# Kernel optimization log

Hardware: AMD Instinct MI355X
Metric: run time of the kernel (lower is better)

## Reference

```python
import jax, jax.numpy as jnp
import numpy as np

N_NODES = 100000
DIM = 256
N_SAMPLES = 64
N_CLASSES = 10


def setup_inputs() -> dict:
    key = jax.random.key(0)
    k1, k2, k3 = jax.random.split(key, 3)
    data = jax.random.normal(k1, (N_SAMPLES, DIM), dtype=jnp.float32)
    V = jax.random.uniform(k2, (N_NODES, DIM), dtype=jnp.float32)  # node matrix (torch.rand init)
    labels = jax.random.randint(k3, (N_SAMPLES,), 0, N_CLASSES)
    return {"data": data, "V": V, "labels": labels, "it": 0}


def reference(data, V, labels, it):
    # SOINN+ per-sample BMU search + BMU/sBMU weight pull, fixed node capacity.
    # eps schedules exactly as in ASOINN.forward.
    eps_b = 1.0 / (it + 2)
    eps_n = 1.0 / ((it + 1) * 100)

    def step(Vc, sample):
        # pairwise L2 distance of sample vs all nodes: [N]
        diff = sample[None, :] - Vc
        dists = jnp.sqrt(jnp.sum(diff * diff, axis=-1) + 1e-12)
        neg_vals, idx = jax.lax.top_k(-dists, 2)  # two smallest
        b, s = idx[0], idx[1]
        # update_bmu: V[b] += eps_b * (sample - V[b]); neighbor pull on sBMU
        Vc = Vc.at[b].add(eps_b * (sample - Vc[b]))
        Vc = Vc.at[s].add(eps_n * (sample - Vc[s]))
        return Vc, -neg_vals  # (b_dist, s_dist)

    V_final, bmu_dists = jax.lax.scan(step, V, data)
    return bmu_dists  # [N_SAMPLES, 2]
```

## Files before the change

### kernel.cpp

```cpp
#include <hip/hip_runtime.h>
#include <math.h>


#define N_NODES 100000
#define DIM     256
#define NS      64
#define NCH     1563
#define KC      32
#define NBMW    3125
#define CAP     4096
#define KL      192
#define KLS     136

typedef unsigned long long u64;

__device__ __forceinline__ u64 pk(float d, int i) {
  return ((u64)__float_as_uint(d) << 32) | (unsigned)i;
}
__device__ __forceinline__ u64 tkey(float d, int slot, int node) {
  return ((u64)__float_as_uint(d) << 32) |
         (u64)(0x80000000u | ((unsigned)slot << 17) | (unsigned)node);
}
__device__ __forceinline__ u64 umin64(u64 a, u64 b) { return a < b ? a : b; }
__device__ __forceinline__ u64 umax64(u64 a, u64 b) { return a > b ? a : b; }
__device__ __forceinline__ void mrg2(u64& A0, u64& A1, u64 B0, u64 B1) {
  u64 m = umax64(A0, B0);
  A0 = umin64(A0, B0);
  A1 = umin64(umin64(A1, B1), m);
}

template <int C>
__device__ __forceinline__ u64 dpp64(u64 x) {
  unsigned lo = (unsigned)__builtin_amdgcn_update_dpp(
      (int)0xFFFFFFFF, (int)(unsigned)(x & 0xFFFFFFFFull), C, 0xF, 0xF, false);
  unsigned hi = (unsigned)__builtin_amdgcn_update_dpp(
      (int)0xFFFFFFFF, (int)(unsigned)(x >> 32), C, 0xF, 0xF, false);
  return ((u64)hi << 32) | lo;
}
template <int C>
__device__ __forceinline__ void dpp_round(u64& A0, u64& A1) {
  u64 B0 = dpp64<C>(A0);
  u64 B1 = dpp64<C>(A1);
  mrg2(A0, A1, B0, B1);
}

__global__ void k_xx(const float* __restrict__ X, float* __restrict__ XX) {
  int i = blockIdx.x, j = threadIdx.x;
  const float* xi = X + i * DIM;
  const float* xj = X + j * DIM;
  float acc = 0.f;
  for (int k = 0; k < DIM; k += 4) {
    float4 a = *(const float4*)(xi + k);
    float4 b = *(const float4*)(xj + k);
    acc += a.x * b.x + a.y * b.y + a.z * b.z + a.w * b.w;
  }
  XX[i * NS + j] = acc;
}

__global__ __launch_bounds__(256) void k_dist(const float* __restrict__ X,
                                              const float* __restrict__ V,
                                              const float* __restrict__ XX,
                                              float* __restrict__ P,
                                              float* __restrict__ PT,
                                              float* __restrict__ Q,
                                              u64* __restrict__ SUMC) {
  __shared__ float Xl[KC][68];
  __shared__ float Vl[KC][132];
  __shared__ float sq[128];
  const int tid = threadIdx.x;
  const int n0  = blockIdx.x * 128;
  const int ty  = tid >> 5;
  const int tx  = tid & 31;
  float acc[8][4];
#pragma unroll
  for (int i = 0; i < 8; i++)
#pragma unroll
    for (int u = 0; u < 4; u++) acc[i][u] = 0.f;
  float qa = 0.f;
  const int xsl = tid & 63;
  const int xkk = (tid >> 6) * 8;
  const int vn  = tid & 127;
  const int vkk = (tid >> 7) * 16;
  const bool vok = (n0 + vn < N_NODES);
  const float* vrow = V + (size_t)(n0 + vn) * DIM + vkk;
  const float* xrow = X + xsl * DIM + xkk;

  float4 xr0, xr1, vr[4];
  xr0 = *(const float4*)(xrow + 0);
  xr1 = *(const float4*)(xrow + 4);
#pragma unroll
  for (int m = 0; m < 4; m++)
    vr[m] = vok ? *(const float4*)(vrow + 4 * m) : make_float4(0.f, 0.f, 0.f, 0.f);

  for (int c = 0; c < 8; c++) {
    __syncthreads();
    Xl[xkk + 0][xsl] = xr0.x; Xl[xkk + 1][xsl] = xr0.y;
    Xl[xkk + 2][xsl] = xr0.z; Xl[xkk + 3][xsl] = xr0.w;
    Xl[xkk + 4][xsl] = xr1.x; Xl[xkk + 5][xsl] = xr1.y;
    Xl[xkk + 6][xsl] = xr1.z; Xl[xkk + 7][xsl] = xr1.w;
#pragma unroll
    for (int m = 0; m < 4; m++) {
      Vl[vkk + 4 * m + 0][vn] = vr[m].x; Vl[vkk + 4 * m + 1][vn] = vr[m].y;
      Vl[vkk + 4 * m + 2][vn] = vr[m].z; Vl[vkk + 4 * m + 3][vn] = vr[m].w;
    }
    __syncthreads();
    if (c + 1 < 8) {
      int kc = (c + 1) * KC;
      xr0 = *(const float4*)(xrow + kc);
      xr1 = *(const float4*)(xrow + kc + 4);
#pragma unroll
      for (int m = 0; m < 4; m++)
        vr[m] = vok ? *(const float4*)(vrow + kc + 4 * m)
                    : make_float4(0.f, 0.f, 0.f, 0.f);
    }
    if (tid < 128) {
      float qq = 0.f;
#pragma unroll 8
      for (int k = 0; k < KC; k++) { float t = Vl[k][tid]; qq += t * t; }
      qa += qq;
    }
#pragma unroll 4
    for (int k = 0; k < KC; k++) {
      float xs[8], vs[4];
      *(float4*)&xs[0] = *(const float4*)&Xl[k][ty * 8];
      *(float4*)&xs[4] = *(const float4*)&Xl[k][ty * 8 + 4];
      *(float4*)&vs[0] = *(const float4*)&Vl[k][tx * 4];
#pragma unroll
      for (int i = 0; i < 8; i++)
#pragma unroll
        for (int u = 0; u < 4; u++) acc[i][u] += xs[i] * vs[u];
    }
  }
  if (tid < 128) sq[tid] = qa;
  __syncthreads();
  if (tid < 128 && n0 + tid < N_NODES) Q[n0 + tid] = qa;
  float qs[4];
  *(float4*)&qs[0] = *(const float4*)&sq[tx * 4];
  const bool full = (n0 + 128) <= N_NODES;
#pragma unroll
  for (int i = 0; i < 8; i++) {
    int s = ty * 8 + i;
    float xn = XX[s * NS + s];
#pragma unroll
    for (int u = 0; u < 4; u++) acc[i][u] = xn - 2.f * acc[i][u] + qs[u];
    float* prow = P + (size_t)s * N_NODES + n0 + tx * 4;
    if (full) {
      *(float4*)(prow) = make_float4(acc[i][0], acc[i][1], acc[i][2], acc[i][3]);
    } else {
#pragma unroll
      for (int u = 0; u < 4; u++) {
        int n = n0 + tx * 4 + u;
        if (n < N_NODES) prow[u] = acc[i][u];
      }
    }
  }
#pragma unroll
  for (int u = 0; u < 4; u++) {
    int n = n0 + tx * 4 + u;
    if (n < N_NODES) {
      float* pt = PT + (size_t)n * NS + ty * 8;
      *(float4*)(pt)     = make_float4(acc[0][u], acc[1][u], acc[2][u], acc[3][u]);
      *(float4*)(pt + 4) = make_float4(acc[4][u], acc[5][u], acc[6][u], acc[7][u]);
    }
  }
#pragma unroll
  for (int i = 0; i < 8; i++) {
    int s = ty * 8 + i;
    u64 key = ~0ull;
#pragma unroll
    for (int u = 0; u < 4; u++) {
      int n = n0 + tx * 4 + u;
      if (n < N_NODES) key = umin64(key, pk(acc[i][u], n));
    }
#pragma unroll
    for (int off = 1; off <= 8; off <<= 1)
      key = umin64(key, (u64)__shfl_xor((unsigned long long)key, off, 64));
    if ((tx & 15) == 0) {
      int chunk = (n0 >> 6) + (tx >> 4);
      if (chunk < NCH) SUMC[(size_t)s * NCH + chunk] = key;
    }
  }
}

__global__ __launch_bounds__(1024) void k_build(const u64* __restrict__ SUMC,
                                                const float* __restrict__ P,
                                                u64* __restrict__ L) {
  __shared__ u64 A[CAP];
  __shared__ u64 Twave[16];
  __shared__ float Tsh;
  __shared__ int cnt;
  const int j = blockIdx.x, tid = threadIdx.x;
  const int w = tid >> 6, l = tid & 63;
  {
    int base = w * 98;
    u64 v0 = (base + l < NCH) ? SUMC[(size_t)j * NCH + base + l] : ~0ull;
    u64 v1 = (l < 34 && base + 64 + l < NCH)
                 ? SUMC[(size_t)j * NCH + base + 64 + l] : ~0ull;
    u64 s9 = ~0ull;
#pragma unroll
    for (int r = 0; r < 9; r++) {
      u64 m = umin64(v0, v1);
#pragma unroll
      for (int off = 1; off <= 32; off <<= 1)
        m = umin64(m, (u64)__shfl_xor((unsigned long long)m, off, 64));
      if (r == 8) { s9 = m; } else {
        if (v0 == m) v0 = ~0ull;
        if (v1 == m) v1 = ~0ull;
      }
    }
    if (l == 0) Twave[w] = s9;
  }
  __syncthreads();
  if (tid == 0) {
    u64 t = 0;
    for (int i = 0; i < 16; i++) t = umax64(t, Twave[i]);
    Tsh = __uint_as_float((unsigned)(t >> 32));
    cnt = 0;
  }
  __syncthreads();
  const float T = Tsh;
  const float* prow = P + (size_t)j * N_NODES;
  for (int n0 = tid * 4; n0 < N_NODES + 3; n0 += 4096) {
    float d[4];
    if (n0 + 3 < N_NODES) {
      float4 p = *(const float4*)(prow + n0);
      d[0] = p.x; d[1] = p.y; d[2] = p.z; d[3] = p.w;
    } else {
#pragma unroll
      for (int e = 0; e < 4; e++)
        d[e] = (n0 + e < N_NODES) ? prow[n0 + e] : INFINITY;
    }
#pragma unroll
    for (int e = 0; e < 4; e++) {
      if (d[e] <= T) {
        int pos = atomicAdd(&cnt, 1);
        if (pos < CAP) A[pos] = pk(d[e], n0 + e);
      }
    }
  }
  __syncthreads();
  int n = cnt; if (n > CAP) n = CAP;
  int M = 256; while (M < n) M <<= 1;
  for (int i = tid; i < M; i += 1024)
    if (i >= n) A[i] = ~0ull;
  __syncthreads();
  for (int k = 2; k <= M; k <<= 1)
    for (int s2 = k >> 1; s2 > 0; s2 >>= 1) {
      for (int i = tid; i < M; i += 1024) {
        int p = i ^ s2;
        if (p > i) {
          u64 a = A[i], b = A[p];
          bool up = ((i & k) == 0);
          if ((a > b) == up) { A[i] = b; A[p] = a; }
        }
      }
      __syncthreads();
    }
  for (int i = tid; i < KLS; i += 1024) L[(size_t)j * KL + i] = A[i];
}

__global__ __launch_bounds__(192) void k_seq(
    const float* __restrict__ PT, const float* __restrict__ Q,
    const float* __restrict__ XXg, const u64* __restrict__ L,
    const int* __restrict__ itp, float* __restrict__ out) {
  __shared__ float XXl[NS * 65];
  __shared__ float g[128][65];
  __shared__ float qv[128];
  __shared__ unsigned int bitmap[NBMW];
  __shared__ int tracked[128];
  __shared__ u64 cand16[NS][16];
  __shared__ float specg[4][6][NS];
  __shared__ float specq[4][6];
  __shared__ int   specid[4][6];
  __shared__ int readyC[NS];
  __shared__ int readyS[NS];
  __shared__ int done[NS];

  const int tid = threadIdx.x;
  const int wv = tid >> 6;
  const int lane = tid & 63;

  for (int i = tid; i < NS * NS; i += 192) {
    int r = i >> 6, c = i & 63;
    XXl[r * 65 + c] = XXg[i];
  }
  for (int i = tid; i < NBMW; i += 192) bitmap[i] = 0u;
  for (int i = tid; i < NS; i += 192) { readyC[i] = 0; readyS[i] = 0; done[i] = 0; }
  __syncthreads();

  const int it = itp[0];
  const float eps_b = 1.0f / (float)(it + 2);
  const float eps_n = 1.0f / (float)((it + 1) * 100);
  const float xdl = XXl[lane * 65 + lane];

  if (wv == 0) {
    int ns = 0;
    int pw0 = -1, pw1 = -1, pw2 = -1, pw3 = -1;
    for (int j = 0; j < NS; j++) {
      while (__hip_atomic_load(&readyC[j], __ATOMIC_ACQUIRE,
                               __HIP_MEMORY_SCOPE_WORKGROUP) == 0)
        __builtin_amdgcn_s_sleep(1);
      const int sb = j & 3;
      u64 ck = (lane < 16) ? cand16[j][lane] : ~0ull;
      float gA = g[lane][j], gB = g[lane + 64][j];
      float qvA = qv[lane],  qvB = qv[lane + 64];
      int   tA = tracked[lane], tB = tracked[lane + 64];
      float xrow = XXl[j * 65 + lane];
      float xnj  = XXl[j * 65 + j];
      u64 A0 = ~0ull, A1 = ~0ull;
      {
        int id = (int)(unsigned)(ck & 0xFFFFFFFFull);
        bool ok = (ck != ~0ull) && id != pw0 && id != pw1 && id != pw2 && id != pw3;
        if (ok) { A0 = ck; }
      }
      if (lane < ns)      { float d = xnj - 2.f * gA + qvA; mrg2(A0, A1, tkey(d, lane, tA), ~0ull); }
      if (lane + 64 < ns) { float d = xnj - 2.f * gB + qvB; mrg2(A0, A1, tkey(d, lane + 64, tB), ~0ull); }
      dpp_round<0x111>(A0, A1);
      dpp_round<0x112>(A0, A1);
      dpp_round<0x114>(A0, A1);
      dpp_round<0x118>(A0, A1);
      dpp_round<0x142>(A0, A1);
      dpp_round<0x143>(A0, A1);
      const unsigned lo0 = (unsigned)__builtin_amdgcn_readlane(
          (int)(unsigned)(A0 & 0xFFFFFFFFull), 63);
      const unsigned lo1 = (unsigned)__builtin_amdgcn_readlane(
          (int)(unsigned)(A1 & 0xFFFFFFFFull), 63);
      const int r0 = (int)(lo0 & 0x1FFFFu);
      const int r1 = (int)(lo1 & 0x1FFFFu);
      const bool new0 = (lo0 & 0x80000000u) == 0u;
      const bool new1 = (lo1 & 0x80000000u) == 0u;
      const int sl0 = new0 ? ns : (int)((lo0 >> 17) & 127u);
      const int sl1 = new1 ? (ns + (new0 ? 1 : 0)) : (int)((lo1 >> 17) & 127u);
      if (lane == 63) {
        float2 o;
        o.x = sqrtf(fmaxf(__uint_as_float((unsigned)(A0 >> 32)), 0.f) + 1e-12f);
        o.y = sqrtf(fmaxf(__uint_as_float((unsigned)(A1 >> 32)), 0.f) + 1e-12f);
        *(float2*)(out + j * 2) = o;
      }
      float gt0 = g[sl0][lane];
      float gt1 = g[sl1][lane];
      while (__hip_atomic_load(&readyS[j], __ATOMIC_ACQUIRE,
                               __HIP_MEMORY_SCOPE_WORKGROUP) == 0)
        __builtin_amdgcn_s_sleep(1);
      float sgv[6], sqv[6]; int sid[6];
#pragma unroll
      for (int s = 0; s < 6; s++) {
        sgv[s] = specg[sb][s][lane];
        sid[s] = specid[sb][s];
        sqv[s] = specq[sb][s];
      }
      bool hit0 = false, hit1 = false;
      float pv0 = 0.f, qq0 = 0.f, pv1 = 0.f, qq1 = 0.f;
#pragma unroll
      for (int s = 0; s < 6; s++) {
        bool h0 = (sid[s] == r0), h1 = (sid[s] == r1);
        pv0 = h0 ? sgv[s] : pv0;  qq0 = h0 ? sqv[s] : qq0;  hit0 |= h0;
        pv1 = h1 ? sgv[s] : pv1;  qq1 = h1 ? sqv[s] : qq1;  hit1 |= h1;
      }
      if (new0 && !hit0) { pv0 = PT[(size_t)r0 * NS + lane]; qq0 = Q[r0]; }
      if (new1 && !hit1) { pv1 = PT[(size_t)r1 * NS + lane]; qq1 = Q[r1]; }
      float gold0 = new0 ? (0.5f * (xdl + qq0 - pv0)) : gt0;
      float qold0 = new0 ? qq0
                         : __uint_as_float((unsigned)__builtin_amdgcn_readlane(
                               (int)__float_as_uint(sl0 < 64 ? qvA : qvB), sl0 & 63));
      float gj0 = __uint_as_float(
          (unsigned)__builtin_amdgcn_readlane((int)__float_as_uint(gold0), j));
      g[sl0][lane] = (1.f - eps_b) * gold0 + eps_b * xrow;
      if (lane == 0) {
        float om = 1.f - eps_b;
        qv[sl0] = om * om * qold0 + 2.f * eps_b * om * gj0 + eps_b * eps_b * xnj;
        tracked[sl0] = r0;
        if (new0) bitmap[r0 >> 5] |= 1u << (r0 & 31);
      }
      float gold1 = new1 ? (0.5f * (xdl + qq1 - pv1)) : gt1;
      float qold1 = new1 ? qq1
                         : __uint_as_float((unsigned)__builtin_amdgcn_readlane(
                               (int)__float_as_uint(sl1 < 64 ? qvA : qvB), sl1 & 63));
      float gj1 = __uint_as_float(
          (unsigned)__builtin_amdgcn_readlane((int)__float_as_uint(gold1), j));
      g[sl1][lane] = (1.f - eps_n) * gold1 + eps_n * xrow;
      if (lane == 0) {
        float on = 1.f - eps_n;
        qv[sl1] = on * on * qold1 + 2.f * eps_n * on * gj1 + eps_n * eps_n * xnj;
        tracked[sl1] = r1;
        if (new1) bitmap[r1 >> 5] |= 1u << (r1 & 31);
      }
      ns += (new0 ? 1 : 0) + (new1 ? 1 : 0);
      pw2 = pw0; pw3 = pw1; pw0 = r0; pw1 = r1;
      __hip_atomic_store(&done[j], 1, __ATOMIC_RELEASE,
                         __HIP_MEMORY_SCOPE_WORKGROUP);
    }
  } else {
    for (int t = (wv == 1 ? 0 : 1); t < NS; t += 2) {
      const u64* Lr = L + (size_t)t * KL;
      u64 e0 = Lr[lane], e1 = Lr[lane + 64];
      u64 e2 = (lane < 8) ? Lr[128 + lane] : ~0ull;
      if (t >= 3) {
        while (__hip_atomic_load(&done[t - 3], __ATOMIC_ACQUIRE,
                                 __HIP_MEMORY_SCOPE_WORKGROUP) == 0)
          __builtin_amdgcn_s_sleep(1);
      }
      int i0 = (int)(unsigned)(e0 & 0xFFFFFFFFull);
      int i1 = (int)(unsigned)(e1 & 0xFFFFFFFFull);
      int i2 = (int)(unsigned)(e2 & 0xFFFFFFFFull);
      bool t0 = (e0 == ~0ull) || ((bitmap[i0 >> 5] >> (i0 & 31)) & 1u);
      bool t1 = (e1 == ~0ull) || ((bitmap[i1 >> 5] >> (i1 & 31)) & 1u);
      bool t2 = (e2 == ~0ull) || ((bitmap[i2 >> 5] >> (i2 & 31)) & 1u);
      u64 um0 = ~__ballot(t0), um1 = ~__ballot(t1), um2 = ~__ballot(t2);
      u64 below = (1ull << lane) - 1;
      int c0n = __popcll((unsigned long long)um0);
      int c1n = __popcll((unsigned long long)um1);
      int rank0 = __popcll((unsigned long long)(um0 & below));
      int rank1 = c0n + __popcll((unsigned long long)(um1 & below));
      int rank2 = c0n + c1n + __popcll((unsigned long long)(um2 & below));
      if (!t0 && rank0 < 16) cand16[t][rank0] = e0;
      if (!t1 && rank1 < 16) cand16[t][rank1] = e1;
      if (!t2 && rank2 < 16) cand16[t][rank2] = e2;
      int U = c0n + c1n + __popcll((unsigned long long)um2);
      if (lane < 16 && lane >= U) cand16[t][lane] = ~0ull;
      __hip_atomic_store(&readyC[t], 1, __ATOMIC_RELEASE,
                         __HIP_MEMORY_SCOPE_WORKGROUP);
      const int sb = t & 3;
      int ids[6];
#pragma unroll
      for (int s = 0; s < 6; s++)
        ids[s] = (int)(unsigned)(cand16[t][s] & 0xFFFFFFFFull);
#pragma unroll
      for (int s = 0; s < 6; s++)
        specg[sb][s][lane] = PT[(size_t)ids[s] * NS + lane];
      if (lane < 6) {
        specid[sb][lane] = ids[lane];
        specq[sb][lane] = Q[ids[lane]];
      }
      __hip_atomic_store(&readyS[t], 1, __ATOMIC_RELEASE,
                         __HIP_MEMORY_SCOPE_WORKGROUP);
    }
  }
}

extern "C" void kernel_launch(void* const* d_in, const int* in_sizes, int n_in,
                              void* d_out, int out_size, void* d_ws, size_t ws_size,
                              hipStream_t stream) {
  const float* X  = (const float*)d_in[0];
  const float* V  = (const float*)d_in[1];
  const int*  itp = (const int*)d_in[3];
  float* out = (float*)d_out;

  char* ws = (char*)d_ws;
  size_t off = 0;
  auto alloc = [&](size_t bytes) -> void* {
    size_t o = (off + 255) & ~(size_t)255;
    off = o + bytes;
    return (void*)(ws + o);
  };
  float* P    = (float*)alloc((size_t)NS * N_NODES * sizeof(float));
  float* PT   = (float*)alloc((size_t)NS * N_NODES * sizeof(float));
  float* Q    = (float*)alloc((size_t)N_NODES * sizeof(float));
  float* XXp  = (float*)alloc((size_t)NS * NS * sizeof(float));
  u64*   SUMC = (u64*)alloc((size_t)NS * NCH * sizeof(u64));
  u64*   Lst  = (u64*)alloc((size_t)NS * KL * sizeof(u64));

  k_xx   <<<NS, NS, 0, stream>>>(X, XXp);
  k_dist <<<(N_NODES + 127) / 128, 256, 0, stream>>>(X, V, XXp, P, PT, Q, SUMC);
  k_build<<<NS, 1024, 0, stream>>>(SUMC, P, Lst);
  k_seq  <<<1, 192, 0, stream>>>(PT, Q, XXp, Lst, itp, out);
}
```

Baseline: 308.1 us.

## Deepen k_seq producer pipeline and keep tracked state in registers

The sequential BMU kernel now uses four producer waves instead of two, with an 8-deep speculation buffer holding 12 prefetched candidate rows instead of 6. The consumer wave keeps per-slot q and tracked ids in registers, and prefetches the next step's g column, forwarding this step's updates by readlane. It also signals done earlier, right after setting the bitmap, so producers can run further ahead. The rank is encoded in the candidate key, so a speculative row is found by direct indexing rather than an id search. The exclusion window grows to 10 previous winners to match the deeper lookahead. The aim is to shorten the serial critical path per sample, at the cost of more shared memory and more complex forwarding logic.

```diff
diff --git a/kernel.cpp b/kernel.cpp
--- a/kernel.cpp
+++ b/kernel.cpp
@@ -28,6 +28,10 @@
   A0 = umin64(A0, B0);
   A1 = umin64(umin64(A1, B1), m);
 }
+__device__ __forceinline__ float rdlane_f(float v, int l) {
+  return __uint_as_float((unsigned)__builtin_amdgcn_readlane(
+      (int)__float_as_uint(v), l));
+}
 
 template <int C>
 __device__ __forceinline__ u64 dpp64(u64 x) {
@@ -43,6 +47,11 @@
   u64 B1 = dpp64<C>(A1);
   mrg2(A0, A1, B0, B1);
 }
+
+#define SPIN(flag)                                                        \
+  while (__hip_atomic_load(&(flag), __ATOMIC_ACQUIRE,                     \
+                           __HIP_MEMORY_SCOPE_WORKGROUP) == 0)            \
+    __builtin_amdgcn_s_sleep(1);
 
 __global__ void k_xx(const float* __restrict__ X, float* __restrict__ XX) {
   int i = blockIdx.x, j = threadIdx.x;
@@ -259,19 +268,16 @@
   for (int i = tid; i < KLS; i += 1024) L[(size_t)j * KL + i] = A[i];
 }
 
-__global__ __launch_bounds__(192) void k_seq(
+__global__ __launch_bounds__(320) void k_seq(
     const float* __restrict__ PT, const float* __restrict__ Q,
     const float* __restrict__ XXg, const u64* __restrict__ L,
     const int* __restrict__ itp, float* __restrict__ out) {
   __shared__ float XXl[NS * 65];
   __shared__ float g[128][65];
-  __shared__ float qv[128];
   __shared__ unsigned int bitmap[NBMW];
-  __shared__ int tracked[128];
   __shared__ u64 cand16[NS][16];
-  __shared__ float specg[4][6][NS];
-  __shared__ float specq[4][6];
-  __shared__ int   specid[4][6];
+  __shared__ float specg[8][12][NS];
+  __shared__ float specq[8][12];
   __shared__ int readyC[NS];
   __shared__ int readyS[NS];
   __shared__ int done[NS];
@@ -280,38 +286,51 @@
   const int wv = tid >> 6;
   const int lane = tid & 63;
 
-  for (int i = tid; i < NS * NS; i += 192) {
+  for (int i = tid; i < NS * NS; i += 320) {
     int r = i >> 6, c = i & 63;
     XXl[r * 65 + c] = XXg[i];
   }
-  for (int i = tid; i < NBMW; i += 192) bitmap[i] = 0u;
-  for (int i = tid; i < NS; i += 192) { readyC[i] = 0; readyS[i] = 0; done[i] = 0; }
+  for (int i = tid; i < NBMW; i += 320) bitmap[i] = 0u;
+  for (int i = tid; i < NS; i += 320) { readyC[i] = 0; readyS[i] = 0; done[i] = 0; }
   __syncthreads();
 
   const int it = itp[0];
   const float eps_b = 1.0f / (float)(it + 2);
   const float eps_n = 1.0f / (float)((it + 1) * 100);
-  const float xdl = XXl[lane * 65 + lane];
 
   if (wv == 0) {
+    const float xdl = XXl[lane * 65 + lane];
+    float gA = 0.f, gB = 0.f;
+    float qvA = 0.f, qvB = 0.f;
+    int tA = 0, tB = 0;
     int ns = 0;
-    int pw0 = -1, pw1 = -1, pw2 = -1, pw3 = -1;
+    int pw[10];
+#pragma unroll
+    for (int k2 = 0; k2 < 10; k2++) pw[k2] = -1;
+
+    SPIN(readyC[0]);
+    SPIN(readyC[1]);
+    u64 ck = (lane < 16) ? cand16[0][lane] : ~0ull;
+    SPIN(readyS[0]);
+
     for (int j = 0; j < NS; j++) {
-      while (__hip_atomic_load(&readyC[j], __ATOMIC_ACQUIRE,
-                               __HIP_MEMORY_SCOPE_WORKGROUP) == 0)
-        __builtin_amdgcn_s_sleep(1);
-      const int sb = j & 3;
-      u64 ck = (lane < 16) ? cand16[j][lane] : ~0ull;
-      float gA = g[lane][j], gB = g[lane + 64][j];
-      float qvA = qv[lane],  qvB = qv[lane + 64];
-      int   tA = tracked[lane], tB = tracked[lane + 64];
-      float xrow = XXl[j * 65 + lane];
-      float xnj  = XXl[j * 65 + j];
+      u64 ckn = ~0ull;
+      float gAn = 0.f, gBn = 0.f;
+      if (j < 63) {
+        if (lane < 16) ckn = cand16[j + 1][lane];
+        gAn = g[lane][j + 1];
+        gBn = g[lane + 64][j + 1];
+      }
+      float xrowv = XXl[j * 65 + lane];
+      const float xnj = rdlane_f(xdl, j);
+
       u64 A0 = ~0ull, A1 = ~0ull;
       {
-        int id = (int)(unsigned)(ck & 0xFFFFFFFFull);
-        bool ok = (ck != ~0ull) && id != pw0 && id != pw1 && id != pw2 && id != pw3;
-        if (ok) { A0 = ck; }
+        int id = (int)((unsigned)ck & 0x1FFFFu);
+        bool ok = (ck != ~0ull);
+#pragma unroll
+        for (int k2 = 0; k2 < 10; k2++) ok = ok && (id != pw[k2]);
+        if (ok) A0 = ck;
       }
       if (lane < ns)      { float d = xnj - 2.f * gA + qvA; mrg2(A0, A1, tkey(d, lane, tA), ~0ull); }
       if (lane + 64 < ns) { float d = xnj - 2.f * gB + qvB; mrg2(A0, A1, tkey(d, lane + 64, tB), ~0ull); }
@@ -331,75 +350,87 @@
       const bool new1 = (lo1 & 0x80000000u) == 0u;
       const int sl0 = new0 ? ns : (int)((lo0 >> 17) & 127u);
       const int sl1 = new1 ? (ns + (new0 ? 1 : 0)) : (int)((lo1 >> 17) & 127u);
+      const int rk0 = (int)((lo0 >> 17) & 15u);
+      const int rk1 = (int)((lo1 >> 17) & 15u);
+
+      float gt0 = g[sl0][lane];
+      float gt1 = g[sl1][lane];
+      const int sb = j & 7;
+      float pv0 = 0.f, qq0 = 0.f, pv1 = 0.f, qq1 = 0.f;
+      if (new0) { pv0 = specg[sb][rk0][lane]; qq0 = specq[sb][rk0]; }
+      if (new1) { pv1 = specg[sb][rk1][lane]; qq1 = specq[sb][rk1]; }
+
+      if (lane == 0) {
+        if (new0) bitmap[r0 >> 5] |= 1u << (r0 & 31);
+        if (new1) bitmap[r1 >> 5] |= 1u << (r1 & 31);
+      }
+      __hip_atomic_store(&done[j], 1, __ATOMIC_RELEASE,
+                         __HIP_MEMORY_SCOPE_WORKGROUP);
+
       if (lane == 63) {
         float2 o;
         o.x = sqrtf(fmaxf(__uint_as_float((unsigned)(A0 >> 32)), 0.f) + 1e-12f);
         o.y = sqrtf(fmaxf(__uint_as_float((unsigned)(A1 >> 32)), 0.f) + 1e-12f);
         *(float2*)(out + j * 2) = o;
       }
-      float gt0 = g[sl0][lane];
-      float gt1 = g[sl1][lane];
-      while (__hip_atomic_load(&readyS[j], __ATOMIC_ACQUIRE,
-                               __HIP_MEMORY_SCOPE_WORKGROUP) == 0)
-        __builtin_amdgcn_s_sleep(1);
-      float sgv[6], sqv[6]; int sid[6];
-#pragma unroll
-      for (int s = 0; s < 6; s++) {
-        sgv[s] = specg[sb][s][lane];
-        sid[s] = specid[sb][s];
-        sqv[s] = specq[sb][s];
-      }
-      bool hit0 = false, hit1 = false;
-      float pv0 = 0.f, qq0 = 0.f, pv1 = 0.f, qq1 = 0.f;
-#pragma unroll
-      for (int s = 0; s < 6; s++) {
-        bool h0 = (sid[s] == r0), h1 = (sid[s] == r1);
-        pv0 = h0 ? sgv[s] : pv0;  qq0 = h0 ? sqv[s] : qq0;  hit0 |= h0;
-        pv1 = h1 ? sgv[s] : pv1;  qq1 = h1 ? sqv[s] : qq1;  hit1 |= h1;
-      }
-      if (new0 && !hit0) { pv0 = PT[(size_t)r0 * NS + lane]; qq0 = Q[r0]; }
-      if (new1 && !hit1) { pv1 = PT[(size_t)r1 * NS + lane]; qq1 = Q[r1]; }
+
+      if (new0 && rk0 >= 12) { pv0 = PT[(size_t)r0 * NS + lane]; qq0 = Q[r0]; }
+      if (new1 && rk1 >= 12) { pv1 = PT[(size_t)r1 * NS + lane]; qq1 = Q[r1]; }
+
       float gold0 = new0 ? (0.5f * (xdl + qq0 - pv0)) : gt0;
-      float qold0 = new0 ? qq0
-                         : __uint_as_float((unsigned)__builtin_amdgcn_readlane(
-                               (int)__float_as_uint(sl0 < 64 ? qvA : qvB), sl0 & 63));
-      float gj0 = __uint_as_float(
-          (unsigned)__builtin_amdgcn_readlane((int)__float_as_uint(gold0), j));
-      g[sl0][lane] = (1.f - eps_b) * gold0 + eps_b * xrow;
-      if (lane == 0) {
-        float om = 1.f - eps_b;
-        qv[sl0] = om * om * qold0 + 2.f * eps_b * om * gj0 + eps_b * eps_b * xnj;
-        tracked[sl0] = r0;
-        if (new0) bitmap[r0 >> 5] |= 1u << (r0 & 31);
-      }
+      float gnew0 = (1.f - eps_b) * gold0 + eps_b * xrowv;
+      g[sl0][lane] = gnew0;
+      float qold0 = new0 ? qq0 : rdlane_f(sl0 < 64 ? qvA : qvB, sl0 & 63);
+      float gj0 = rdlane_f(gold0, j);
+      float om = 1.f - eps_b;
+      float qn0 = om * om * qold0 + 2.f * eps_b * om * gj0 + eps_b * eps_b * xnj;
+
       float gold1 = new1 ? (0.5f * (xdl + qq1 - pv1)) : gt1;
-      float qold1 = new1 ? qq1
-                         : __uint_as_float((unsigned)__builtin_amdgcn_readlane(
-                               (int)__float_as_uint(sl1 < 64 ? qvA : qvB), sl1 & 63));
-      float gj1 = __uint_as_float(
-          (unsigned)__builtin_amdgcn_readlane((int)__float_as_uint(gold1), j));
-      g[sl1][lane] = (1.f - eps_n) * gold1 + eps_n * xrow;
-      if (lane == 0) {
-        float on = 1.f - eps_n;
-        qv[sl1] = on * on * qold1 + 2.f * eps_n * on * gj1 + eps_n * eps_n * xnj;
-        tracked[sl1] = r1;
-        if (new1) bitmap[r1 >> 5] |= 1u << (r1 & 31);
-      }
+      float gnew1 = (1.f - eps_n) * gold1 + eps_n * xrowv;
+      g[sl1][lane] = gnew1;
+      float qold1 = new1 ? qq1 : rdlane_f(sl1 < 64 ? qvA : qvB, sl1 & 63);
+      float gj1 = rdlane_f(gold1, j);
+      float on = 1.f - eps_n;
+      float qn1 = on * on * qold1 + 2.f * eps_n * on * gj1 + eps_n * eps_n * xnj;
+
+      if (sl0 < 64) { if (lane == sl0)      { qvA = qn0; tA = r0; } }
+      else          { if (lane == sl0 - 64) { qvB = qn0; tB = r0; } }
+      if (sl1 < 64) { if (lane == sl1)      { qvA = qn1; tA = r1; } }
+      else          { if (lane == sl1 - 64) { qvB = qn1; tB = r1; } }
+
+      if (j < 63) {
+        float xnext = rdlane_f(xrowv, j + 1);
+        float xd1 = rdlane_f(xdl, j + 1);
+        float goldn0 = new0 ? (0.5f * (xd1 + qq0 - rdlane_f(pv0, j + 1)))
+                            : rdlane_f(sl0 < 64 ? gAn : gBn, sl0 & 63);
+        float gp0 = (1.f - eps_b) * goldn0 + eps_b * xnext;
+        float goldn1 = new1 ? (0.5f * (xd1 + qq1 - rdlane_f(pv1, j + 1)))
+                            : rdlane_f(sl1 < 64 ? gAn : gBn, sl1 & 63);
+        float gp1 = (1.f - eps_n) * goldn1 + eps_n * xnext;
+        if (sl0 < 64) { if (lane == sl0)      gAn = gp0; }
+        else          { if (lane == sl0 - 64) gBn = gp0; }
+        if (sl1 < 64) { if (lane == sl1)      gAn = gp1; }
+        else          { if (lane == sl1 - 64) gBn = gp1; }
+        gA = gAn; gB = gBn;
+      }
+
       ns += (new0 ? 1 : 0) + (new1 ? 1 : 0);
-      pw2 = pw0; pw3 = pw1; pw0 = r0; pw1 = r1;
-      __hip_atomic_store(&done[j], 1, __ATOMIC_RELEASE,
-                         __HIP_MEMORY_SCOPE_WORKGROUP);
+#pragma unroll
+      for (int k2 = 9; k2 >= 2; k2--) pw[k2] = pw[k2 - 2];
+      pw[0] = r0; pw[1] = r1;
+
+      if (j < 63) {
+        SPIN(readyS[j + 1]);
+        if (j < 62) SPIN(readyC[j + 2]);
+        ck = ckn;
+      }
     }
   } else {
-    for (int t = (wv == 1 ? 0 : 1); t < NS; t += 2) {
+    for (int t = wv - 1; t < NS; t += 4) {
       const u64* Lr = L + (size_t)t * KL;
       u64 e0 = Lr[lane], e1 = Lr[lane + 64];
       u64 e2 = (lane < 8) ? Lr[128 + lane] : ~0ull;
-      if (t >= 3) {
-        while (__hip_atomic_load(&done[t - 3], __ATOMIC_ACQUIRE,
-                                 __HIP_MEMORY_SCOPE_WORKGROUP) == 0)
-          __builtin_amdgcn_s_sleep(1);
-      }
+      if (t >= 6) { SPIN(done[t - 6]); }
       int i0 = (int)(unsigned)(e0 & 0xFFFFFFFFull);
       int i1 = (int)(unsigned)(e1 & 0xFFFFFFFFull);
       int i2 = (int)(unsigned)(e2 & 0xFFFFFFFFull);
@@ -413,25 +444,24 @@
       int rank0 = __popcll((unsigned long long)(um0 & below));
       int rank1 = c0n + __popcll((unsigned long long)(um1 & below));
       int rank2 = c0n + c1n + __popcll((unsigned long long)(um2 & below));
-      if (!t0 && rank0 < 16) cand16[t][rank0] = e0;
-      if (!t1 && rank1 < 16) cand16[t][rank1] = e1;
-      if (!t2 && rank2 < 16) cand16[t][rank2] = e2;
+      if (!t0 && rank0 < 16) cand16[t][rank0] = e0 | ((u64)(unsigned)rank0 << 17);
+      if (!t1 && rank1 < 16) cand16[t][rank1] = e1 | ((u64)(unsigned)rank1 << 17);
+      if (!t2 && rank2 < 16) cand16[t][rank2] = e2 | ((u64)(unsigned)rank2 << 17);
       int U = c0n + c1n + __popcll((unsigned long long)um2);
       if (lane < 16 && lane >= U) cand16[t][lane] = ~0ull;
       __hip_atomic_store(&readyC[t], 1, __ATOMIC_RELEASE,
                          __HIP_MEMORY_SCOPE_WORKGROUP);
-      const int sb = t & 3;
-      int ids[6];
-#pragma unroll
-      for (int s = 0; s < 6; s++)
-        ids[s] = (int)(unsigned)(cand16[t][s] & 0xFFFFFFFFull);
-#pragma unroll
-      for (int s = 0; s < 6; s++)
+      const int sb = t & 7;
+      int ids[12];
+#pragma unroll
+      for (int s = 0; s < 12; s++) {
+        u64 e = cand16[t][s];
+        ids[s] = (e == ~0ull) ? 0 : (int)((unsigned)e & 0x1FFFFu);
+      }
+#pragma unroll
+      for (int s = 0; s < 12; s++)
         specg[sb][s][lane] = PT[(size_t)ids[s] * NS + lane];
-      if (lane < 6) {
-        specid[sb][lane] = ids[lane];
-        specq[sb][lane] = Q[ids[lane]];
-      }
+      if (lane < 12) specq[sb][lane] = Q[ids[lane]];
       __hip_atomic_store(&readyS[t], 1, __ATOMIC_RELEASE,
                          __HIP_MEMORY_SCOPE_WORKGROUP);
     }
@@ -463,5 +493,5 @@
   k_xx   <<<NS, NS, 0, stream>>>(X, XXp);
   k_dist <<<(N_NODES + 127) / 128, 256, 0, stream>>>(X, V, XXp, P, PT, Q, SUMC);
   k_build<<<NS, 1024, 0, stream>>>(SUMC, P, Lst);
-  k_seq  <<<1, 192, 0, stream>>>(PT, Q, XXp, Lst, itp, out);
-}
+  k_seq  <<<1, 320, 0, stream>>>(PT, Q, XXp, Lst, itp, out);
+}
```

Measured after the change: 329.9 us. 1.07x slower.

## Encode candidate rank in key and signal done earlier in sequential loop

Applied to the files above, without the earlier changes.

The serial wave now reads each candidate's prefetch slot straight from bits packed into its key, instead of matching ids against the speculative slots. This drops the specid table and the separate readyC flag in favour of one readyS wait. The done flag is published right after the bitmap update, so helper waves can start filtering sooner. Next-iteration shared loads are hoisted to the end of the loop, and xnj now comes from a readlane. The risk is that the rank bits overlap node-id bits when ids are masked to 17 bits, and that waiting on readyS makes the serial wave stall on the PT prefetch.

```diff
diff --git a/kernel.cpp b/kernel.cpp
--- a/kernel.cpp
+++ b/kernel.cpp
@@ -28,6 +28,10 @@
   A0 = umin64(A0, B0);
   A1 = umin64(umin64(A1, B1), m);
 }
+__device__ __forceinline__ float rdlane_f(float v, int l) {
+  return __uint_as_float((unsigned)__builtin_amdgcn_readlane(
+      (int)__float_as_uint(v), l));
+}
 
 template <int C>
 __device__ __forceinline__ u64 dpp64(u64 x) {
@@ -43,6 +47,11 @@
   u64 B1 = dpp64<C>(A1);
   mrg2(A0, A1, B0, B1);
 }
+
+#define SPIN(flag)                                                        \
+  while (__hip_atomic_load(&(flag), __ATOMIC_ACQUIRE,                     \
+                           __HIP_MEMORY_SCOPE_WORKGROUP) == 0)            \
+    __builtin_amdgcn_s_sleep(1);
 
 __global__ void k_xx(const float* __restrict__ X, float* __restrict__ XX) {
   int i = blockIdx.x, j = threadIdx.x;
@@ -271,8 +280,6 @@
   __shared__ u64 cand16[NS][16];
   __shared__ float specg[4][6][NS];
   __shared__ float specq[4][6];
-  __shared__ int   specid[4][6];
-  __shared__ int readyC[NS];
   __shared__ int readyS[NS];
   __shared__ int done[NS];
 
@@ -285,7 +292,7 @@
     XXl[r * 65 + c] = XXg[i];
   }
   for (int i = tid; i < NBMW; i += 192) bitmap[i] = 0u;
-  for (int i = tid; i < NS; i += 192) { readyC[i] = 0; readyS[i] = 0; done[i] = 0; }
+  for (int i = tid; i < NS; i += 192) { readyS[i] = 0; done[i] = 0; }
   __syncthreads();
 
   const int it = itp[0];
@@ -296,22 +303,20 @@
   if (wv == 0) {
     int ns = 0;
     int pw0 = -1, pw1 = -1, pw2 = -1, pw3 = -1;
+    SPIN(readyS[0]);
+    u64 ck = (lane < 16) ? cand16[0][lane] : ~0ull;
+    float gA = g[lane][0], gB = g[lane + 64][0];
+    float qvA = qv[lane], qvB = qv[lane + 64];
+    int tA = tracked[lane], tB = tracked[lane + 64];
+    float xrow = XXl[0 * 65 + lane];
+
     for (int j = 0; j < NS; j++) {
-      while (__hip_atomic_load(&readyC[j], __ATOMIC_ACQUIRE,
-                               __HIP_MEMORY_SCOPE_WORKGROUP) == 0)
-        __builtin_amdgcn_s_sleep(1);
-      const int sb = j & 3;
-      u64 ck = (lane < 16) ? cand16[j][lane] : ~0ull;
-      float gA = g[lane][j], gB = g[lane + 64][j];
-      float qvA = qv[lane],  qvB = qv[lane + 64];
-      int   tA = tracked[lane], tB = tracked[lane + 64];
-      float xrow = XXl[j * 65 + lane];
-      float xnj  = XXl[j * 65 + j];
+      const float xnj = rdlane_f(xdl, j);
       u64 A0 = ~0ull, A1 = ~0ull;
       {
-        int id = (int)(unsigned)(ck & 0xFFFFFFFFull);
+        int id = (int)((unsigned)ck & 0x1FFFFu);
         bool ok = (ck != ~0ull) && id != pw0 && id != pw1 && id != pw2 && id != pw3;
-        if (ok) { A0 = ck; }
+        if (ok) A0 = ck;
       }
       if (lane < ns)      { float d = xnj - 2.f * gA + qvA; mrg2(A0, A1, tkey(d, lane, tA), ~0ull); }
       if (lane + 64 < ns) { float d = xnj - 2.f * gB + qvB; mrg2(A0, A1, tkey(d, lane + 64, tB), ~0ull); }
@@ -331,75 +336,69 @@
       const bool new1 = (lo1 & 0x80000000u) == 0u;
       const int sl0 = new0 ? ns : (int)((lo0 >> 17) & 127u);
       const int sl1 = new1 ? (ns + (new0 ? 1 : 0)) : (int)((lo1 >> 17) & 127u);
+      const int rk0 = (int)((lo0 >> 17) & 15u);
+      const int rk1 = (int)((lo1 >> 17) & 15u);
+
+      const int sb = j & 3;
+      float gt0 = g[sl0][lane];
+      float gt1 = g[sl1][lane];
+      float pv0 = 0.f, qq0 = 0.f, pv1 = 0.f, qq1 = 0.f;
+      if (new0) { pv0 = specg[sb][rk0][lane]; qq0 = specq[sb][rk0]; }
+      if (new1) { pv1 = specg[sb][rk1][lane]; qq1 = specq[sb][rk1]; }
+
+      if (lane == 0) {
+        if (new0) bitmap[r0 >> 5] |= 1u << (r0 & 31);
+        if (new1) bitmap[r1 >> 5] |= 1u << (r1 & 31);
+      }
+      __hip_atomic_store(&done[j], 1, __ATOMIC_RELEASE,
+                         __HIP_MEMORY_SCOPE_WORKGROUP);
+
       if (lane == 63) {
         float2 o;
         o.x = sqrtf(fmaxf(__uint_as_float((unsigned)(A0 >> 32)), 0.f) + 1e-12f);
         o.y = sqrtf(fmaxf(__uint_as_float((unsigned)(A1 >> 32)), 0.f) + 1e-12f);
         *(float2*)(out + j * 2) = o;
       }
-      float gt0 = g[sl0][lane];
-      float gt1 = g[sl1][lane];
-      while (__hip_atomic_load(&readyS[j], __ATOMIC_ACQUIRE,
-                               __HIP_MEMORY_SCOPE_WORKGROUP) == 0)
-        __builtin_amdgcn_s_sleep(1);
-      float sgv[6], sqv[6]; int sid[6];
-#pragma unroll
-      for (int s = 0; s < 6; s++) {
-        sgv[s] = specg[sb][s][lane];
-        sid[s] = specid[sb][s];
-        sqv[s] = specq[sb][s];
-      }
-      bool hit0 = false, hit1 = false;
-      float pv0 = 0.f, qq0 = 0.f, pv1 = 0.f, qq1 = 0.f;
-#pragma unroll
-      for (int s = 0; s < 6; s++) {
-        bool h0 = (sid[s] == r0), h1 = (sid[s] == r1);
-        pv0 = h0 ? sgv[s] : pv0;  qq0 = h0 ? sqv[s] : qq0;  hit0 |= h0;
-        pv1 = h1 ? sgv[s] : pv1;  qq1 = h1 ? sqv[s] : qq1;  hit1 |= h1;
-      }
-      if (new0 && !hit0) { pv0 = PT[(size_t)r0 * NS + lane]; qq0 = Q[r0]; }
-      if (new1 && !hit1) { pv1 = PT[(size_t)r1 * NS + lane]; qq1 = Q[r1]; }
+
+      if (new0 && rk0 >= 6) { pv0 = PT[(size_t)r0 * NS + lane]; qq0 = Q[r0]; }
+      if (new1 && rk1 >= 6) { pv1 = PT[(size_t)r1 * NS + lane]; qq1 = Q[r1]; }
+
       float gold0 = new0 ? (0.5f * (xdl + qq0 - pv0)) : gt0;
-      float qold0 = new0 ? qq0
-                         : __uint_as_float((unsigned)__builtin_amdgcn_readlane(
-                               (int)__float_as_uint(sl0 < 64 ? qvA : qvB), sl0 & 63));
-      float gj0 = __uint_as_float(
-          (unsigned)__builtin_amdgcn_readlane((int)__float_as_uint(gold0), j));
       g[sl0][lane] = (1.f - eps_b) * gold0 + eps_b * xrow;
+      float qold0 = new0 ? qq0 : rdlane_f(sl0 < 64 ? qvA : qvB, sl0 & 63);
+      float gj0 = rdlane_f(gold0, j);
       if (lane == 0) {
         float om = 1.f - eps_b;
         qv[sl0] = om * om * qold0 + 2.f * eps_b * om * gj0 + eps_b * eps_b * xnj;
         tracked[sl0] = r0;
-        if (new0) bitmap[r0 >> 5] |= 1u << (r0 & 31);
       }
       float gold1 = new1 ? (0.5f * (xdl + qq1 - pv1)) : gt1;
-      float qold1 = new1 ? qq1
-                         : __uint_as_float((unsigned)__builtin_amdgcn_readlane(
-                               (int)__float_as_uint(sl1 < 64 ? qvA : qvB), sl1 & 63));
-      float gj1 = __uint_as_float(
-          (unsigned)__builtin_amdgcn_readlane((int)__float_as_uint(gold1), j));
       g[sl1][lane] = (1.f - eps_n) * gold1 + eps_n * xrow;
+      float qold1 = new1 ? qq1 : rdlane_f(sl1 < 64 ? qvA : qvB, sl1 & 63);
+      float gj1 = rdlane_f(gold1, j);
       if (lane == 0) {
         float on = 1.f - eps_n;
         qv[sl1] = on * on * qold1 + 2.f * eps_n * on * gj1 + eps_n * eps_n * xnj;
         tracked[sl1] = r1;
-        if (new1) bitmap[r1 >> 5] |= 1u << (r1 & 31);
       }
       ns += (new0 ? 1 : 0) + (new1 ? 1 : 0);
       pw2 = pw0; pw3 = pw1; pw0 = r0; pw1 = r1;
-      __hip_atomic_store(&done[j], 1, __ATOMIC_RELEASE,
-                         __HIP_MEMORY_SCOPE_WORKGROUP);
+
+      if (j < 63) {
+        SPIN(readyS[j + 1]);
+        ck = (lane < 16) ? cand16[j + 1][lane] : ~0ull;
+        gA = g[lane][j + 1]; gB = g[lane + 64][j + 1];
+        qvA = qv[lane]; qvB = qv[lane + 64];
+        tA = tracked[lane]; tB = tracked[lane + 64];
+        xrow = XXl[(j + 1) * 65 + lane];
+      }
     }
   } else {
     for (int t = (wv == 1 ? 0 : 1); t < NS; t += 2) {
       const u64* Lr = L + (size_t)t * KL;
       u64 e0 = Lr[lane], e1 = Lr[lane + 64];
       u64 e2 = (lane < 8) ? Lr[128 + lane] : ~0ull;
-      if (t >= 3) {
-        while (__hip_atomic_load(&done[t - 3], __ATOMIC_ACQUIRE,
-                                 __HIP_MEMORY_SCOPE_WORKGROUP) == 0)
-          __builtin_amdgcn_s_sleep(1);
-      }
+      if (t >= 3) { SPIN(done[t - 3]); }
       int i0 = (int)(unsigned)(e0 & 0xFFFFFFFFull);
       int i1 = (int)(unsigned)(e1 & 0xFFFFFFFFull);
       int i2 = (int)(unsigned)(e2 & 0xFFFFFFFFull);
@@ -413,25 +412,20 @@
       int rank0 = __popcll((unsigned long long)(um0 & below));
       int rank1 = c0n + __popcll((unsigned long long)(um1 & below));
       int rank2 = c0n + c1n + __popcll((unsigned long long)(um2 & below));
-      if (!t0 && rank0 < 16) cand16[t][rank0] = e0;
-      if (!t1 && rank1 < 16) cand16[t][rank1] = e1;
-      if (!t2 && rank2 < 16) cand16[t][rank2] = e2;
+      if (!t0 && rank0 < 16) cand16[t][rank0] = e0 | ((u64)(unsigned)rank0 << 17);
+      if (!t1 && rank1 < 16) cand16[t][rank1] = e1 | ((u64)(unsigned)rank1 << 17);
+      if (!t2 && rank2 < 16) cand16[t][rank2] = e2 | ((u64)(unsigned)rank2 << 17);
       int U = c0n + c1n + __popcll((unsigned long long)um2);
       if (lane < 16 && lane >= U) cand16[t][lane] = ~0ull;
-      __hip_atomic_store(&readyC[t], 1, __ATOMIC_RELEASE,
-                         __HIP_MEMORY_SCOPE_WORKGROUP);
       const int sb = t & 3;
       int ids[6];
 #pragma unroll
       for (int s = 0; s < 6; s++)
-        ids[s] = (int)(unsigned)(cand16[t][s] & 0xFFFFFFFFull);
+        ids[s] = (int)((unsigned)cand16[t][s] & 0x1FFFFu);
 #pragma unroll
       for (int s = 0; s < 6; s++)
         specg[sb][s][lane] = PT[(size_t)ids[s] * NS + lane];
-      if (lane < 6) {
-        specid[sb][lane] = ids[lane];
-        specq[sb][lane] = Q[ids[lane]];
-      }
+      if (lane < 6) specq[sb][lane] = Q[ids[lane]];
       __hip_atomic_store(&readyS[t], 1, __ATOMIC_RELEASE,
                          __HIP_MEMORY_SCOPE_WORKGROUP);
     }
```

After: 309.6 us. Within noise of the previous version (+0.5%).

## Halve distance-kernel node tile and use packed FP32 FMA inner loop

Applied to the files above, without the earlier changes.

The distance GEMM block now covers 64 nodes instead of 128, so each thread computes an 8x2 tile and the grid doubles to 1563 blocks. The inner product uses inline v_pk_fma_f32 with op_sel to broadcast sample values, so one instruction performs two FMAs. The V tile load is reorganized so four threads cover each node row, and the chunk-min reduction now spans a full 32-lane group, with one SUMC entry written per block. The aim is more blocks for occupancy across the MI355X CUs plus higher FMA throughput. The cost is lower data reuse per thread and more shared-memory traffic per FLOP.

```diff
diff --git a/kernel.cpp b/kernel.cpp
--- a/kernel.cpp
+++ b/kernel.cpp
@@ -13,6 +13,7 @@
 #define KLS     136
 
 typedef unsigned long long u64;
+typedef __attribute__((ext_vector_type(2))) float f32x2;
 
 __device__ __forceinline__ u64 pk(float d, int i) {
   return ((u64)__float_as_uint(d) << 32) | (unsigned)i;
@@ -27,6 +28,15 @@
   u64 m = umax64(A0, B0);
   A0 = umin64(A0, B0);
   A1 = umin64(umin64(A1, B1), m);
+}
+
+__device__ __forceinline__ void pkfma_lo(f32x2& acc, f32x2 xp, f32x2 vp) {
+  asm("v_pk_fma_f32 %0, %1, %2, %0 op_sel:[0,0,0] op_sel_hi:[0,1,1]"
+      : "+v"(acc) : "v"(xp), "v"(vp));
+}
+__device__ __forceinline__ void pkfma_hi(f32x2& acc, f32x2 xp, f32x2 vp) {
+  asm("v_pk_fma_f32 %0, %1, %2, %0 op_sel:[1,0,0] op_sel_hi:[1,1,1]"
+      : "+v"(acc) : "v"(xp), "v"(vp));
 }
 
 template <int C>
@@ -65,32 +75,29 @@
                                               float* __restrict__ Q,
                                               u64* __restrict__ SUMC) {
   __shared__ float Xl[KC][68];
-  __shared__ float Vl[KC][132];
-  __shared__ float sq[128];
+  __shared__ float Vl[KC][66];
+  __shared__ float sq[64];
   const int tid = threadIdx.x;
-  const int n0  = blockIdx.x * 128;
+  const int n0  = blockIdx.x * 64;
   const int ty  = tid >> 5;
   const int tx  = tid & 31;
-  float acc[8][4];
-#pragma unroll
-  for (int i = 0; i < 8; i++)
-#pragma unroll
-    for (int u = 0; u < 4; u++) acc[i][u] = 0.f;
+  f32x2 acc2[8];
+#pragma unroll
+  for (int i = 0; i < 8; i++) { acc2[i][0] = 0.f; acc2[i][1] = 0.f; }
   float qa = 0.f;
   const int xsl = tid & 63;
   const int xkk = (tid >> 6) * 8;
-  const int vn  = tid & 127;
-  const int vkk = (tid >> 7) * 16;
-  const bool vok = (n0 + vn < N_NODES);
-  const float* vrow = V + (size_t)(n0 + vn) * DIM + vkk;
+  const int vrw = tid >> 2;
+  const int vkk = (tid & 3) * 8;
+  const bool vok = (n0 + vrw < N_NODES);
+  const float* vrow = V + (size_t)(n0 + vrw) * DIM + vkk;
   const float* xrow = X + xsl * DIM + xkk;
 
-  float4 xr0, xr1, vr[4];
+  float4 xr0, xr1, vr0, vr1;
   xr0 = *(const float4*)(xrow + 0);
   xr1 = *(const float4*)(xrow + 4);
-#pragma unroll
-  for (int m = 0; m < 4; m++)
-    vr[m] = vok ? *(const float4*)(vrow + 4 * m) : make_float4(0.f, 0.f, 0.f, 0.f);
+  vr0 = vok ? *(const float4*)(vrow + 0) : make_float4(0.f, 0.f, 0.f, 0.f);
+  vr1 = vok ? *(const float4*)(vrow + 4) : make_float4(0.f, 0.f, 0.f, 0.f);
 
   for (int c = 0; c < 8; c++) {
     __syncthreads();
@@ -98,22 +105,19 @@
     Xl[xkk + 2][xsl] = xr0.z; Xl[xkk + 3][xsl] = xr0.w;
     Xl[xkk + 4][xsl] = xr1.x; Xl[xkk + 5][xsl] = xr1.y;
     Xl[xkk + 6][xsl] = xr1.z; Xl[xkk + 7][xsl] = xr1.w;
-#pragma unroll
-    for (int m = 0; m < 4; m++) {
-      Vl[vkk + 4 * m + 0][vn] = vr[m].x; Vl[vkk + 4 * m + 1][vn] = vr[m].y;
-      Vl[vkk + 4 * m + 2][vn] = vr[m].z; Vl[vkk + 4 * m + 3][vn] = vr[m].w;
-    }
+    Vl[vkk + 0][vrw] = vr0.x; Vl[vkk + 1][vrw] = vr0.y;
+    Vl[vkk + 2][vrw] = vr0.z; Vl[vkk + 3][vrw] = vr0.w;
+    Vl[vkk + 4][vrw] = vr1.x; Vl[vkk + 5][vrw] = vr1.y;
+    Vl[vkk + 6][vrw] = vr1.z; Vl[vkk + 7][vrw] = vr1.w;
     __syncthreads();
     if (c + 1 < 8) {
       int kc = (c + 1) * KC;
       xr0 = *(const float4*)(xrow + kc);
       xr1 = *(const float4*)(xrow + kc + 4);
-#pragma unroll
-      for (int m = 0; m < 4; m++)
-        vr[m] = vok ? *(const float4*)(vrow + kc + 4 * m)
-                    : make_float4(0.f, 0.f, 0.f, 0.f);
-    }
-    if (tid < 128) {
+      vr0 = vok ? *(const float4*)(vrow + kc) : make_float4(0.f, 0.f, 0.f, 0.f);
+      vr1 = vok ? *(const float4*)(vrow + kc + 4) : make_float4(0.f, 0.f, 0.f, 0.f);
+    }
+    if (tid < 64) {
       float qq = 0.f;
 #pragma unroll 8
       for (int k = 0; k < KC; k++) { float t = Vl[k][tid]; qq += t * t; }
@@ -121,42 +125,53 @@
     }
 #pragma unroll 4
     for (int k = 0; k < KC; k++) {
-      float xs[8], vs[4];
-      *(float4*)&xs[0] = *(const float4*)&Xl[k][ty * 8];
-      *(float4*)&xs[4] = *(const float4*)&Xl[k][ty * 8 + 4];
-      *(float4*)&vs[0] = *(const float4*)&Vl[k][tx * 4];
-#pragma unroll
-      for (int i = 0; i < 8; i++)
-#pragma unroll
-        for (int u = 0; u < 4; u++) acc[i][u] += xs[i] * vs[u];
-    }
-  }
-  if (tid < 128) sq[tid] = qa;
-  __syncthreads();
-  if (tid < 128 && n0 + tid < N_NODES) Q[n0 + tid] = qa;
-  float qs[4];
-  *(float4*)&qs[0] = *(const float4*)&sq[tx * 4];
-  const bool full = (n0 + 128) <= N_NODES;
+      float4 xa = *(const float4*)&Xl[k][ty * 8];
+      float4 xb = *(const float4*)&Xl[k][ty * 8 + 4];
+      f32x2 vp = *(const f32x2*)&Vl[k][tx * 2];
+      f32x2 xp0, xp1, xp2, xp3;
+      xp0[0] = xa.x; xp0[1] = xa.y;
+      xp1[0] = xa.z; xp1[1] = xa.w;
+      xp2[0] = xb.x; xp2[1] = xb.y;
+      xp3[0] = xb.z; xp3[1] = xb.w;
+      pkfma_lo(acc2[0], xp0, vp);
+      pkfma_hi(acc2[1], xp0, vp);
+      pkfma_lo(acc2[2], xp1, vp);
+      pkfma_hi(acc2[3], xp1, vp);
+      pkfma_lo(acc2[4], xp2, vp);
+      pkfma_hi(acc2[5], xp2, vp);
+      pkfma_lo(acc2[6], xp3, vp);
+      pkfma_hi(acc2[7], xp3, vp);
+    }
+  }
+  float acc[8][2];
+#pragma unroll
+  for (int i = 0; i < 8; i++) { acc[i][0] = acc2[i][0]; acc[i][1] = acc2[i][1]; }
+  if (tid < 64) sq[tid] = qa;
+  __syncthreads();
+  if (tid < 64 && n0 + tid < N_NODES) Q[n0 + tid] = qa;
+  float qs[2];
+  *(f32x2*)&qs[0] = *(const f32x2*)&sq[tx * 2];
+  const bool full = (n0 + 64) <= N_NODES;
 #pragma unroll
   for (int i = 0; i < 8; i++) {
     int s = ty * 8 + i;
     float xn = XX[s * NS + s];
 #pragma unroll
-    for (int u = 0; u < 4; u++) acc[i][u] = xn - 2.f * acc[i][u] + qs[u];
-    float* prow = P + (size_t)s * N_NODES + n0 + tx * 4;
+    for (int u = 0; u < 2; u++) acc[i][u] = xn - 2.f * acc[i][u] + qs[u];
+    float* prow = P + (size_t)s * N_NODES + n0 + tx * 2;
     if (full) {
-      *(float4*)(prow) = make_float4(acc[i][0], acc[i][1], acc[i][2], acc[i][3]);
+      *(float2*)(prow) = make_float2(acc[i][0], acc[i][1]);
     } else {
 #pragma unroll
-      for (int u = 0; u < 4; u++) {
-        int n = n0 + tx * 4 + u;
+      for (int u = 0; u < 2; u++) {
+        int n = n0 + tx * 2 + u;
         if (n < N_NODES) prow[u] = acc[i][u];
       }
     }
   }
 #pragma unroll
-  for (int u = 0; u < 4; u++) {
-    int n = n0 + tx * 4 + u;
+  for (int u = 0; u < 2; u++) {
+    int n = n0 + tx * 2 + u;
     if (n < N_NODES) {
       float* pt = PT + (size_t)n * NS + ty * 8;
       *(float4*)(pt)     = make_float4(acc[0][u], acc[1][u], acc[2][u], acc[3][u]);
@@ -168,17 +183,14 @@
     int s = ty * 8 + i;
     u64 key = ~0ull;
 #pragma unroll
-    for (int u = 0; u < 4; u++) {
-      int n = n0 + tx * 4 + u;
+    for (int u = 0; u < 2; u++) {
+      int n = n0 + tx * 2 + u;
       if (n < N_NODES) key = umin64(key, pk(acc[i][u], n));
     }
 #pragma unroll
-    for (int off = 1; off <= 8; off <<= 1)
+    for (int off = 1; off <= 16; off <<= 1)
       key = umin64(key, (u64)__shfl_xor((unsigned long long)key, off, 64));
-    if ((tx & 15) == 0) {
-      int chunk = (n0 >> 6) + (tx >> 4);
-      if (chunk < NCH) SUMC[(size_t)s * NCH + chunk] = key;
-    }
+    if (tx == 0) SUMC[(size_t)s * NCH + blockIdx.x] = key;
   }
 }
 
@@ -461,7 +473,7 @@
   u64*   Lst  = (u64*)alloc((size_t)NS * KL * sizeof(u64));
 
   k_xx   <<<NS, NS, 0, stream>>>(X, XXp);
-  k_dist <<<(N_NODES + 127) / 128, 256, 0, stream>>>(X, V, XXp, P, PT, Q, SUMC);
+  k_dist <<<(N_NODES + 63) / 64, 256, 0, stream>>>(X, V, XXp, P, PT, Q, SUMC);
   k_build<<<NS, 1024, 0, stream>>>(SUMC, P, Lst);
   k_seq  <<<1, 192, 0, stream>>>(PT, Q, XXp, Lst, itp, out);
 }
```

After: 307.4 us, median of 2. Within noise of the previous version (-0.2%).
